# Kernel tuning notes

Hardware: AMD Instinct MI355X
Metric: run time of the kernel (lower is better)

Reference implementation:

```python
import jax, jax.numpy as jnp
import numpy as np

N = 100000  # nodes


def gcn_conv(x, src, dst, deg_inv_sqrt, W, b):
    h = x @ W  # transform first (smaller feature dim for propagation when F_out < F_in)
    norm = deg_inv_sqrt[src] * deg_inv_sqrt[dst]  # [E]
    msg = h[src] * norm[:, None]  # gather + scale
    return jax.ops.segment_sum(msg, dst, num_segments=N) + b


def setup_inputs() -> dict:
    key = jax.random.key(0)
    k1, k2, k3, k4, k5 = jax.random.split(key, 5)
    E = 3200000
    x = jax.random.normal(k1, (N, 512), dtype=jnp.float32)
    edge_index = jax.random.randint(k2, (2, E), 0, N, dtype=jnp.int64)
    W1 = jax.random.normal(k3, (512, 16), dtype=jnp.float32) * (1.0 / np.sqrt(512))
    b1 = jnp.zeros((16,), dtype=jnp.float32)
    W2 = jax.random.normal(k4, (16, 64), dtype=jnp.float32) * (1.0 / np.sqrt(16))
    b2 = jnp.zeros((64,), dtype=jnp.float32)
    return {"x": x, "edge_index": edge_index, "W1": W1, "b1": b1, "W2": W2, "b2": b2}


def reference(x, edge_index, W1, b1, W2, b2):
    # add self-loops (PyG GCNConv default add_self_loops=True)
    loops = jnp.arange(N, dtype=edge_index.dtype)
    src = jnp.concatenate([edge_index[0], loops])
    dst = jnp.concatenate([edge_index[1], loops])
    # symmetric normalization: deg computed on destination (in-degree incl. self-loop)
    deg = jax.ops.segment_sum(jnp.ones_like(dst, dtype=x.dtype), dst, num_segments=N)
    deg_inv_sqrt = jnp.where(deg > 0, jax.lax.rsqrt(jnp.maximum(deg, 1.0)), 0.0)

    h = jax.nn.relu(gcn_conv(x, src, dst, deg_inv_sqrt, W1, b1))
    out = gcn_conv(h, src, dst, deg_inv_sqrt, W2, b2)
    return jax.nn.log_softmax(out, axis=1)
```

## Files before the change

### kernel.cpp

```cpp
#include <hip/hip_runtime.h>

#define FIN 512
#define FMID 16
#define FOUT 64

typedef __attribute__((ext_vector_type(8))) short bf8_t;
typedef __attribute__((ext_vector_type(4))) float f32x4_t;

__device__ __forceinline__ unsigned short f2bf_rne(float f) {
  unsigned u = __float_as_uint(f);
  return (unsigned short)((u + 0x7FFFu + ((u >> 16) & 1u)) >> 16);
}
__device__ __forceinline__ float bf2f(unsigned short h) {
  return __uint_as_float(((unsigned)h) << 16);
}


__global__ void k_count(const int* __restrict__ dst, int* __restrict__ cnt,
                        int* __restrict__ rank, int E) {
  int t = blockIdx.x * blockDim.x + threadIdx.x;
  int e = t * 8;
  if (e + 7 < E) {
    int4 d0 = *(const int4*)(dst + e);
    int4 d1 = *(const int4*)(dst + e + 4);
    int r0 = atomicAdd(&cnt[d0.x], 1);
    int r1 = atomicAdd(&cnt[d0.y], 1);
    int r2 = atomicAdd(&cnt[d0.z], 1);
    int r3 = atomicAdd(&cnt[d0.w], 1);
    int r4 = atomicAdd(&cnt[d1.x], 1);
    int r5 = atomicAdd(&cnt[d1.y], 1);
    int r6 = atomicAdd(&cnt[d1.z], 1);
    int r7 = atomicAdd(&cnt[d1.w], 1);
    *(int4*)(rank + e)     = make_int4(r0, r1, r2, r3);
    *(int4*)(rank + e + 4) = make_int4(r4, r5, r6, r7);
  } else {
    for (; e < E; ++e) rank[e] = atomicAdd(&cnt[dst[e]], 1);
  }
}

__global__ __launch_bounds__(256) void k_blocksum(const int* __restrict__ cnt,
                                                  int* __restrict__ bsum, int n) {
  __shared__ int sm[4];
  int i = blockIdx.x * 256 + threadIdx.x;
  int v = (i < n) ? cnt[i] : 0;
#pragma unroll
  for (int off = 32; off >= 1; off >>= 1) v += __shfl_xor(v, off);
  if ((threadIdx.x & 63) == 0) sm[threadIdx.x >> 6] = v;
  __syncthreads();
  if (threadIdx.x == 0) bsum[blockIdx.x] = sm[0] + sm[1] + sm[2] + sm[3];
}

__global__ __launch_bounds__(512) void k_scanb(int* __restrict__ bsum, int nb) {
  __shared__ int sm[512];
  int t = threadIdx.x;
  int v = (t < nb) ? bsum[t] : 0;
  sm[t] = v;
  __syncthreads();
  for (int off = 1; off < 512; off <<= 1) {
    int add = (t >= off) ? sm[t - off] : 0;
    __syncthreads();
    sm[t] += add;
    __syncthreads();
  }
  if (t < nb) bsum[t] = sm[t] - v;
}

__global__ __launch_bounds__(256) void k_scanf(const int* __restrict__ cnt,
                                               const int* __restrict__ bsum,
                                               int* __restrict__ rowstart,
                                               float* __restrict__ dis, int n) {
  __shared__ int sm[256];
  int t = threadIdx.x;
  int i = blockIdx.x * 256 + t;
  int v = (i < n) ? cnt[i] : 0;
  sm[t] = v;
  __syncthreads();
  for (int off = 1; off < 256; off <<= 1) {
    int add = (t >= off) ? sm[t - off] : 0;
    __syncthreads();
    sm[t] += add;
    __syncthreads();
  }
  int excl = sm[t] - v + bsum[blockIdx.x];
  if (i < n) {
    rowstart[i] = excl;
    dis[i] = rsqrtf((float)v + 1.0f);
  }
  if (i == n - 1) rowstart[n] = excl + v;
}

__global__ void k_scatter(const int* __restrict__ src, const int* __restrict__ dst,
                          const int* __restrict__ rank, const int* __restrict__ rowstart,
                          int* __restrict__ csr_src, int E) {
  int t = blockIdx.x * blockDim.x + threadIdx.x;
  int e = t * 4;
  if (e + 3 < E) {
    int4 s = *(const int4*)(src + e);
    int4 d = *(const int4*)(dst + e);
    int4 r = *(const int4*)(rank + e);
    csr_src[rowstart[d.x] + r.x] = s.x;
    csr_src[rowstart[d.y] + r.y] = s.y;
    csr_src[rowstart[d.z] + r.z] = s.z;
    csr_src[rowstart[d.w] + r.w] = s.w;
  } else {
    for (; e < E; ++e) csr_src[rowstart[dst[e]] + rank[e]] = src[e];
  }
}


__global__ __launch_bounds__(256) void k_gemm1(const float* __restrict__ x,
                                               const float* __restrict__ W1,
                                               const float* __restrict__ dis,
                                               float* __restrict__ hs, int n,
                                               int ntiles) {
  __shared__ short wb_hi[16][64][8];
  __shared__ short wb_lo[16][64][8];
  for (int e = threadIdx.x; e < FIN * FMID; e += 256) {
    int k = e >> 4, j = e & 15;
    int ks = k >> 5, kk = k & 31;
    int L = ((kk >> 3) << 4) + j, i = kk & 7;
    float f = W1[e];
    unsigned short h = f2bf_rne(f);
    wb_hi[ks][L][i] = (short)h;
    wb_lo[ks][L][i] = (short)f2bf_rne(f - bf2f(h));
  }
  __syncthreads();
  const int lane = threadIdx.x & 63;
  const int wid  = threadIdx.x >> 6;
  const int rloc = lane & 15;
  const int q    = lane >> 4;
  for (int tile = blockIdx.x * 4 + wid; tile < ntiles; tile += gridDim.x * 4) {
    int row = tile * 16 + rloc;
    const float4* xr = (const float4*)(x + (size_t)(row < n ? row : n - 1) * FIN);
    f32x4_t acc = {0.f, 0.f, 0.f, 0.f};
#pragma unroll 4
    for (int ks = 0; ks < 16; ++ks) {
      float4 v0 = xr[ks * 8 + q * 2];
      float4 v1 = xr[ks * 8 + q * 2 + 1];
      float fv[8] = {v0.x, v0.y, v0.z, v0.w, v1.x, v1.y, v1.z, v1.w};
      bf8_t ah, al;
#pragma unroll
      for (int i = 0; i < 8; ++i) {
        unsigned short h = f2bf_rne(fv[i]);
        ah[i] = (short)h;
        al[i] = (short)f2bf_rne(fv[i] - bf2f(h));
      }
      bf8_t bh = *(const bf8_t*)&wb_hi[ks][lane][0];
      bf8_t bl = *(const bf8_t*)&wb_lo[ks][lane][0];
      acc = __builtin_amdgcn_mfma_f32_16x16x32_bf16(ah, bh, acc, 0, 0, 0);
      acc = __builtin_amdgcn_mfma_f32_16x16x32_bf16(al, bh, acc, 0, 0, 0);
      acc = __builtin_amdgcn_mfma_f32_16x16x32_bf16(ah, bl, acc, 0, 0, 0);
    }
    int nb = tile * 16 + q * 4;
#pragma unroll
    for (int r = 0; r < 4; ++r) {
      int node = nb + r;
      if (node < n) hs[(size_t)node * FMID + rloc] = acc[r] * dis[node];
    }
  }
}

template <bool RELU>
__global__ __launch_bounds__(256) void k_prop_csr(const float* __restrict__ hs,
                                                  const int* __restrict__ rowstart,
                                                  const int* __restrict__ csr,
                                                  const float* __restrict__ dis,
                                                  const float* __restrict__ bias,
                                                  float* __restrict__ outp, int n) {
  int t = blockIdx.x * blockDim.x + threadIdx.x;
  int node = t >> 4;
  if (node >= n) return;
  const int j = t & 15;
  const int g = j >> 2;
  const int c = j & 3;
  int beg = rowstart[node], end = rowstart[node + 1];
  float4 acc = make_float4(0.f, 0.f, 0.f, 0.f);
  if (g == 0) {
    float4 v = ((const float4*)(hs + (size_t)node * FMID))[c];
    acc.x += v.x; acc.y += v.y; acc.z += v.z; acc.w += v.w;
  }
  int i = beg;
  int stop = beg + ((end - beg) & ~15);
  for (; i < stop; i += 16) {
    int sv = csr[i + j];
#pragma unroll
    for (int k = 0; k < 4; ++k) {
      int sidx = __shfl(sv, k * 4 + g, 16);
      float4 v = ((const float4*)(hs + (size_t)sidx * FMID))[c];
      acc.x += v.x; acc.y += v.y; acc.z += v.z; acc.w += v.w;
    }
  }
  for (int u = 0; i < end; ++i, ++u) {
    int sidx = csr[i];
    if (g == (u & 3)) {
      float4 v = ((const float4*)(hs + (size_t)sidx * FMID))[c];
      acc.x += v.x; acc.y += v.y; acc.z += v.z; acc.w += v.w;
    }
  }
#pragma unroll
  for (int off = 4; off <= 8; off <<= 1) {
    acc.x += __shfl_xor(acc.x, off, 16);
    acc.y += __shfl_xor(acc.y, off, 16);
    acc.z += __shfl_xor(acc.z, off, 16);
    acc.w += __shfl_xor(acc.w, off, 16);
  }
  if (g == 0) {
    float dd = dis[node];
    float4 r;
    r.x = dd * acc.x; r.y = dd * acc.y; r.z = dd * acc.z; r.w = dd * acc.w;
    if (RELU) {
      float4 bb = ((const float4*)bias)[c];
      r.x = fmaxf(r.x + bb.x, 0.f) * dd;
      r.y = fmaxf(r.y + bb.y, 0.f) * dd;
      r.z = fmaxf(r.z + bb.z, 0.f) * dd;
      r.w = fmaxf(r.w + bb.w, 0.f) * dd;
    }
    ((float4*)(outp + (size_t)node * FMID))[c] = r;
  }
}

__global__ __launch_bounds__(256) void k_out(const float* __restrict__ a2,
                                             const float* __restrict__ W2,
                                             const float* __restrict__ b2,
                                             float* __restrict__ out, int n) {
  __shared__ float w[FMID * FOUT];
  for (int idx = threadIdx.x; idx < FMID * FOUT; idx += 256) w[idx] = W2[idx];
  __syncthreads();
  const int lane = threadIdx.x & 63;
  const int node = blockIdx.x * 4 + (threadIdx.x >> 6);
  if (node >= n) return;
  const float* ar = a2 + (size_t)node * FMID;
  float o = b2[lane];
#pragma unroll
  for (int k = 0; k < FMID; ++k) o += ar[k] * w[k * FOUT + lane];
  float m = o;
#pragma unroll
  for (int off = 32; off >= 1; off >>= 1) m = fmaxf(m, __shfl_xor(m, off));
  float e = __expf(o - m);
  float s = e;
#pragma unroll
  for (int off = 32; off >= 1; off >>= 1) s += __shfl_xor(s, off);
  out[(size_t)node * FOUT + lane] = o - m - __logf(s);
}


__global__ void k_deg_init(float* __restrict__ deg, int n) {
  int i = blockIdx.x * blockDim.x + threadIdx.x;
  if (i < n) deg[i] = 1.0f;
}
__global__ void k_deg_edges(const int* __restrict__ dst, float* __restrict__ deg, int E) {
  int e = blockIdx.x * blockDim.x + threadIdx.x;
  if (e < E) atomicAdd(&deg[dst[e]], 1.0f);
}
__global__ void k_deg_finish(float* __restrict__ deg, int n) {
  int i = blockIdx.x * blockDim.x + threadIdx.x;
  if (i < n) deg[i] = rsqrtf(deg[i]);
}
__global__ void k_selfloop_s(const float* __restrict__ hs, const float* __restrict__ dis,
                             float* __restrict__ a, int total16) {
  int t = blockIdx.x * blockDim.x + threadIdx.x;
  if (t < total16) a[t] = hs[t] * dis[t >> 4];
}
__global__ void k_prop_atomic(const float* __restrict__ hs, const int* __restrict__ src,
                              const int* __restrict__ dst, const float* __restrict__ dis,
                              float* __restrict__ outp, int E) {
  int t = blockIdx.x * blockDim.x + threadIdx.x;
  int e = t >> 4;
  if (e >= E) return;
  int jj = t & 15;
  int s = src[e], d = dst[e];
  atomicAdd(&outp[(size_t)d * FMID + jj], hs[(size_t)s * FMID + jj] * dis[d]);
}
__global__ void k_bias_relu_s(float* __restrict__ a, const float* __restrict__ b,
                              const float* __restrict__ dis, int total16) {
  int t = blockIdx.x * blockDim.x + threadIdx.x;
  if (t < total16) {
    float v = a[t] + b[t & 15];
    a[t] = (v > 0.f ? v : 0.f) * dis[t >> 4];
  }
}


extern "C" void kernel_launch(void* const* d_in, const int* in_sizes, int n_in,
                              void* d_out, int out_size, void* d_ws, size_t ws_size,
                              hipStream_t stream) {
  const float* x  = (const float*)d_in[0];
  const int* edge = (const int*)d_in[1];
  const float* W1 = (const float*)d_in[2];
  const float* b1 = (const float*)d_in[3];
  const float* W2 = (const float*)d_in[4];
  const float* b2 = (const float*)d_in[5];
  float* out = (float*)d_out;

  const int N = in_sizes[0] / FIN;
  const int E = in_sizes[1] / 2;
  const int* src = edge;
  const int* dst = edge + E;

  const int T = 256;
  const int t16n = N * FMID;
  const int ntiles = (N + 15) / 16;
  int gblocks = (ntiles + 3) / 4;
  if (gblocks > 2048) gblocks = 2048;

  size_t need_csr = ((size_t)33 * N + (size_t)3 * N + 1 + 512 + (size_t)E) * 4;

  if (ws_size >= need_csr) {
    float* fbase = (float*)d_ws;
    float* dis  = fbase;
    float* buf0 = fbase + (size_t)N;
    float* buf1 = fbase + 17 * (size_t)N;
    int* rank     = (int*)(fbase + (size_t)N);
    int* ibase    = (int*)(fbase + 33 * (size_t)N);
    int* cnt      = ibase;
    int* rowstart = ibase + N;
    int* bsum     = ibase + 3 * (size_t)N + 1;
    int* csr      = ibase + 3 * (size_t)N + 1 + 512;

    const int NB = (N + 255) / 256;

    hipMemsetAsync(cnt, 0, (size_t)N * sizeof(int), stream);
    k_count   <<<((E + 7) / 8 + T - 1) / T, T, 0, stream>>>(dst, cnt, rank, E);
    k_blocksum<<<NB, 256, 0, stream>>>(cnt, bsum, N);
    k_scanb   <<<1, 512, 0, stream>>>(bsum, NB);
    k_scanf   <<<NB, 256, 0, stream>>>(cnt, bsum, rowstart, dis, N);
    k_scatter <<<((E + 3) / 4 + T - 1) / T, T, 0, stream>>>(src, dst, rank, rowstart, csr, E);

    k_gemm1   <<<gblocks, T, 0, stream>>>(x, W1, dis, buf0, N, ntiles);

    const int PB = (t16n + T - 1) / T;
    k_prop_csr<true>  <<<PB, T, 0, stream>>>(buf0, rowstart, csr, dis, b1, buf1, N);
    k_prop_csr<false> <<<PB, T, 0, stream>>>(buf1, rowstart, csr, dis, b1, buf0, N);
    k_out     <<<(N + 3) / 4, T, 0, stream>>>(buf0, W2, b2, out, N);
  } else {
    float* f   = (float*)d_ws;
    float* dis = f;
    float* hs  = f + (size_t)N;
    float* a1  = f + 17 * (size_t)N;
    float* a2  = f + 33 * (size_t)N;
    const long te = (long)E * FMID;

    k_deg_init  <<<(N + T - 1) / T, T, 0, stream>>>(dis, N);
    k_deg_edges <<<(E + T - 1) / T, T, 0, stream>>>(dst, dis, E);
    k_deg_finish<<<(N + T - 1) / T, T, 0, stream>>>(dis, N);

    k_gemm1     <<<gblocks, T, 0, stream>>>(x, W1, dis, hs, N, ntiles);

    k_selfloop_s<<<(t16n + T - 1) / T, T, 0, stream>>>(hs, dis, a1, t16n);
    k_prop_atomic<<<(int)((te + T - 1) / T), T, 0, stream>>>(hs, src, dst, dis, a1, E);
    k_bias_relu_s<<<(t16n + T - 1) / T, T, 0, stream>>>(a1, b1, dis, t16n);

    k_selfloop_s<<<(t16n + T - 1) / T, T, 0, stream>>>(a1, dis, a2, t16n);
    k_prop_atomic<<<(int)((te + T - 1) / T), T, 0, stream>>>(a1, src, dst, dis, a2, E);

    k_out       <<<(N + 3) / 4, T, 0, stream>>>(a2, W2, b2, out, N);
  }
}
```

Measured before the change: 665.3 us.

## Build CSR with two-level bucket sort instead of global atomic counting

Replaces the global-atomic count/rank, three-kernel scan and random scatter with a two-pass bucket sort. Edges are first bucketed by dst>>8 using shared-memory histograms and packed as (src<<8 | dst&255). Each bucket is then sorted locally in shared memory to produce rowstart, dis and the CSR. This cuts contended global atomics and random global writes, in exchange for an extra pass over the edges and guard conditions on N and E. The order of sources within a row may change, which alters the floating-point summation order.

```diff
diff --git a/kernel.cpp b/kernel.cpp
--- a/kernel.cpp
+++ b/kernel.cpp
@@ -16,94 +16,142 @@
 }
 
 
-__global__ void k_count(const int* __restrict__ dst, int* __restrict__ cnt,
-                        int* __restrict__ rank, int E) {
-  int t = blockIdx.x * blockDim.x + threadIdx.x;
-  int e = t * 8;
-  if (e + 7 < E) {
-    int4 d0 = *(const int4*)(dst + e);
-    int4 d1 = *(const int4*)(dst + e + 4);
-    int r0 = atomicAdd(&cnt[d0.x], 1);
-    int r1 = atomicAdd(&cnt[d0.y], 1);
-    int r2 = atomicAdd(&cnt[d0.z], 1);
-    int r3 = atomicAdd(&cnt[d0.w], 1);
-    int r4 = atomicAdd(&cnt[d1.x], 1);
-    int r5 = atomicAdd(&cnt[d1.y], 1);
-    int r6 = atomicAdd(&cnt[d1.z], 1);
-    int r7 = atomicAdd(&cnt[d1.w], 1);
-    *(int4*)(rank + e)     = make_int4(r0, r1, r2, r3);
-    *(int4*)(rank + e + 4) = make_int4(r4, r5, r6, r7);
-  } else {
-    for (; e < E; ++e) rank[e] = atomicAdd(&cnt[dst[e]], 1);
-  }
-}
-
-__global__ __launch_bounds__(256) void k_blocksum(const int* __restrict__ cnt,
-                                                  int* __restrict__ bsum, int n) {
-  __shared__ int sm[4];
-  int i = blockIdx.x * 256 + threadIdx.x;
-  int v = (i < n) ? cnt[i] : 0;
-#pragma unroll
-  for (int off = 32; off >= 1; off >>= 1) v += __shfl_xor(v, off);
-  if ((threadIdx.x & 63) == 0) sm[threadIdx.x >> 6] = v;
-  __syncthreads();
-  if (threadIdx.x == 0) bsum[blockIdx.x] = sm[0] + sm[1] + sm[2] + sm[3];
-}
-
-__global__ __launch_bounds__(512) void k_scanb(int* __restrict__ bsum, int nb) {
-  __shared__ int sm[512];
+#define CHUNK 8192
+
+__global__ __launch_bounds__(256) void k_bhist(const int* __restrict__ dst,
+                                               int* __restrict__ gtot, int E, int nbuck) {
+  __shared__ int hist[1024];
+  const int t = threadIdx.x;
+  const int base = blockIdx.x * CHUNK;
+  const int nloc = min(CHUNK, E - base);
+  for (int i = t; i < nbuck; i += 256) hist[i] = 0;
+  __syncthreads();
+  const int nv = nloc & ~3;
+  for (int i = t * 4; i < nv; i += 1024) {
+    int4 d = *(const int4*)(dst + base + i);
+    atomicAdd(&hist[d.x >> 8], 1);
+    atomicAdd(&hist[d.y >> 8], 1);
+    atomicAdd(&hist[d.z >> 8], 1);
+    atomicAdd(&hist[d.w >> 8], 1);
+  }
+  if (t == 0)
+    for (int i = nv; i < nloc; ++i) atomicAdd(&hist[dst[base + i] >> 8], 1);
+  __syncthreads();
+  for (int i = t; i < nbuck; i += 256) {
+    int c = hist[i];
+    if (c) atomicAdd(&gtot[i], c);
+  }
+}
+
+__global__ __launch_bounds__(1024) void k_bscan(int* __restrict__ gbase,
+                                                int* __restrict__ gcur,
+                                                int* __restrict__ rowstart,
+                                                int E, int n, int nbuck) {
+  __shared__ int sm[1024];
   int t = threadIdx.x;
-  int v = (t < nb) ? bsum[t] : 0;
+  int v = (t < nbuck) ? gbase[t] : 0;
   sm[t] = v;
   __syncthreads();
-  for (int off = 1; off < 512; off <<= 1) {
-    int add = (t >= off) ? sm[t - off] : 0;
+  for (int off = 1; off < 1024; off <<= 1) {
+    int a = (t >= off) ? sm[t - off] : 0;
     __syncthreads();
-    sm[t] += add;
+    sm[t] += a;
     __syncthreads();
   }
-  if (t < nb) bsum[t] = sm[t] - v;
-}
-
-__global__ __launch_bounds__(256) void k_scanf(const int* __restrict__ cnt,
-                                               const int* __restrict__ bsum,
-                                               int* __restrict__ rowstart,
-                                               float* __restrict__ dis, int n) {
-  __shared__ int sm[256];
-  int t = threadIdx.x;
-  int i = blockIdx.x * 256 + t;
-  int v = (i < n) ? cnt[i] : 0;
-  sm[t] = v;
+  int excl = sm[t] - v;
+  if (t < nbuck) {
+    gbase[t] = excl;
+    gcur[t] = excl;
+  }
+  if (t == 0) {
+    gbase[nbuck] = E;
+    rowstart[n] = E;
+  }
+}
+
+__global__ __launch_bounds__(256) void k_bucketA(const int* __restrict__ src,
+                                                 const int* __restrict__ dst,
+                                                 int* __restrict__ gcur,
+                                                 int* __restrict__ packed,
+                                                 int E, int nbuck) {
+  __shared__ int hist[1024];
+  const int t = threadIdx.x;
+  const int base = blockIdx.x * CHUNK;
+  const int nloc = min(CHUNK, E - base);
+  for (int i = t; i < nbuck; i += 256) hist[i] = 0;
+  __syncthreads();
+  const int nv = nloc & ~3;
+  for (int i = t * 4; i < nv; i += 1024) {
+    int4 d = *(const int4*)(dst + base + i);
+    atomicAdd(&hist[d.x >> 8], 1);
+    atomicAdd(&hist[d.y >> 8], 1);
+    atomicAdd(&hist[d.z >> 8], 1);
+    atomicAdd(&hist[d.w >> 8], 1);
+  }
+  if (t == 0)
+    for (int i = nv; i < nloc; ++i) atomicAdd(&hist[dst[base + i] >> 8], 1);
+  __syncthreads();
+  for (int i = t; i < nbuck; i += 256) {
+    int c = hist[i];
+    hist[i] = c ? atomicAdd(&gcur[i], c) : 0;
+  }
+  __syncthreads();
+  for (int i = t * 4; i < nv; i += 1024) {
+    int4 d = *(const int4*)(dst + base + i);
+    int4 s = *(const int4*)(src + base + i);
+    int p0 = atomicAdd(&hist[d.x >> 8], 1);
+    int p1 = atomicAdd(&hist[d.y >> 8], 1);
+    int p2 = atomicAdd(&hist[d.z >> 8], 1);
+    int p3 = atomicAdd(&hist[d.w >> 8], 1);
+    packed[p0] = (s.x << 8) | (d.x & 255);
+    packed[p1] = (s.y << 8) | (d.y & 255);
+    packed[p2] = (s.z << 8) | (d.z & 255);
+    packed[p3] = (s.w << 8) | (d.w & 255);
+  }
+  if (t == 0)
+    for (int i = nv; i < nloc; ++i) {
+      int d = dst[base + i], s = src[base + i];
+      int p = atomicAdd(&hist[d >> 8], 1);
+      packed[p] = (s << 8) | (d & 255);
+    }
+}
+
+__global__ __launch_bounds__(256) void k_bucketB(const int* __restrict__ packed,
+                                                 const int* __restrict__ gbase,
+                                                 int* __restrict__ rowstart,
+                                                 float* __restrict__ dis,
+                                                 int* __restrict__ csr, int n) {
+  __shared__ int cnt[256];
+  __shared__ int cur[256];
+  const int b = blockIdx.x;
+  const int t = threadIdx.x;
+  const int beg = gbase[b], end = gbase[b + 1];
+  cnt[t] = 0;
+  __syncthreads();
+  for (int i = beg + t; i < end; i += 256) atomicAdd(&cnt[packed[i] & 255], 1);
+  __syncthreads();
+  int v = cnt[t];
+  cur[t] = v;
   __syncthreads();
   for (int off = 1; off < 256; off <<= 1) {
-    int add = (t >= off) ? sm[t - off] : 0;
+    int a = (t >= off) ? cur[t - off] : 0;
     __syncthreads();
-    sm[t] += add;
+    cur[t] += a;
     __syncthreads();
   }
-  int excl = sm[t] - v + bsum[blockIdx.x];
-  if (i < n) {
-    rowstart[i] = excl;
-    dis[i] = rsqrtf((float)v + 1.0f);
-  }
-  if (i == n - 1) rowstart[n] = excl + v;
-}
-
-__global__ void k_scatter(const int* __restrict__ src, const int* __restrict__ dst,
-                          const int* __restrict__ rank, const int* __restrict__ rowstart,
-                          int* __restrict__ csr_src, int E) {
-  int t = blockIdx.x * blockDim.x + threadIdx.x;
-  int e = t * 4;
-  if (e + 3 < E) {
-    int4 s = *(const int4*)(src + e);
-    int4 d = *(const int4*)(dst + e);
-    int4 r = *(const int4*)(rank + e);
-    csr_src[rowstart[d.x] + r.x] = s.x;
-    csr_src[rowstart[d.y] + r.y] = s.y;
-    csr_src[rowstart[d.z] + r.z] = s.z;
-    csr_src[rowstart[d.w] + r.w] = s.w;
-  } else {
-    for (; e < E; ++e) csr_src[rowstart[dst[e]] + rank[e]] = src[e];
+  int excl = cur[t] - v;
+  int node = (b << 8) + t;
+  if (node < n) {
+    rowstart[node] = beg + excl;
+    dis[node] = rsqrtf((float)v + 1.0f);
+  }
+  __syncthreads();
+  cur[t] = beg + excl;
+  __syncthreads();
+  for (int i = beg + t; i < end; i += 256) {
+    int p = packed[i];
+    int pos = atomicAdd(&cur[p & 255], 1);
+    csr[pos] = p >> 8;
   }
 }
 
@@ -303,35 +351,38 @@
   int gblocks = (ntiles + 3) / 4;
   if (gblocks > 2048) gblocks = 2048;
 
-  size_t need_csr = ((size_t)33 * N + (size_t)3 * N + 1 + 512 + (size_t)E) * 4;
-
-  if (ws_size >= need_csr) {
+  const int nbuck = (N + 255) >> 8;
+  const int nblkA = (E + CHUNK - 1) / CHUNK;
+
+  size_t need_csr = ((size_t)33 * N + (size_t)(N + 1) + (size_t)(2 * nbuck + 1) +
+                     (size_t)E) * 4;
+  bool new_ok = (ws_size >= need_csr) && ((size_t)E <= (size_t)32 * N) &&
+                (nbuck <= 1024) && ((size_t)N < (1u << 23));
+
+  if (new_ok) {
     float* fbase = (float*)d_ws;
     float* dis  = fbase;
     float* buf0 = fbase + (size_t)N;
     float* buf1 = fbase + 17 * (size_t)N;
-    int* rank     = (int*)(fbase + (size_t)N);
+    int* packed   = (int*)buf0;
     int* ibase    = (int*)(fbase + 33 * (size_t)N);
-    int* cnt      = ibase;
-    int* rowstart = ibase + N;
-    int* bsum     = ibase + 3 * (size_t)N + 1;
-    int* csr      = ibase + 3 * (size_t)N + 1 + 512;
-
-    const int NB = (N + 255) / 256;
-
-    hipMemsetAsync(cnt, 0, (size_t)N * sizeof(int), stream);
-    k_count   <<<((E + 7) / 8 + T - 1) / T, T, 0, stream>>>(dst, cnt, rank, E);
-    k_blocksum<<<NB, 256, 0, stream>>>(cnt, bsum, N);
-    k_scanb   <<<1, 512, 0, stream>>>(bsum, NB);
-    k_scanf   <<<NB, 256, 0, stream>>>(cnt, bsum, rowstart, dis, N);
-    k_scatter <<<((E + 3) / 4 + T - 1) / T, T, 0, stream>>>(src, dst, rank, rowstart, csr, E);
-
-    k_gemm1   <<<gblocks, T, 0, stream>>>(x, W1, dis, buf0, N, ntiles);
+    int* rowstart = ibase;
+    int* gbase    = ibase + (size_t)N + 1;
+    int* gcur     = gbase + nbuck + 1;
+    int* csr      = gcur + nbuck;
+
+    hipMemsetAsync(gbase, 0, (size_t)(nbuck + 1) * sizeof(int), stream);
+    k_bhist  <<<nblkA, T, 0, stream>>>(dst, gbase, E, nbuck);
+    k_bscan  <<<1, 1024, 0, stream>>>(gbase, gcur, rowstart, E, N, nbuck);
+    k_bucketA<<<nblkA, T, 0, stream>>>(src, dst, gcur, packed, E, nbuck);
+    k_bucketB<<<nbuck, T, 0, stream>>>(packed, gbase, rowstart, dis, csr, N);
+
+    k_gemm1  <<<gblocks, T, 0, stream>>>(x, W1, dis, buf0, N, ntiles);
 
     const int PB = (t16n + T - 1) / T;
     k_prop_csr<true>  <<<PB, T, 0, stream>>>(buf0, rowstart, csr, dis, b1, buf1, N);
     k_prop_csr<false> <<<PB, T, 0, stream>>>(buf1, rowstart, csr, dis, b1, buf0, N);
-    k_out     <<<(N + 3) / 4, T, 0, stream>>>(buf0, W2, b2, out, N);
+    k_out    <<<(N + 3) / 4, T, 0, stream>>>(buf0, W2, b2, out, N);
   } else {
     float* f   = (float*)d_ws;
     float* dis = f;
```

After: 548.6 us. 17.5% less time.
